# Kernel tuning notes

Hardware: AMD Instinct MI355X
Metric: run time of the kernel (lower is better)

Reference implementation:

```python
import jax, jax.numpy as jnp
import numpy as np

B, N, F_, H, K_IN, K = 2, 768, 128, 128, 2, 2
TAU = 0.66


def setup_inputs() -> dict:
    key = jax.random.key(0)
    ks = jax.random.split(key, 8)
    s = lambda fan: 1.0 / np.sqrt(fan)
    X = jax.random.normal(ks[0], (B, N, F_), jnp.float32)
    # edge_feat RezeroMLP: Linear(F,H) -> act -> Linear(H,H)
    ef_w1 = jax.random.normal(ks[1], (F_, H), jnp.float32) * s(F_)
    ef_b1 = jnp.zeros((H,), jnp.float32)
    ef_w2 = jax.random.normal(ks[2], (H, H), jnp.float32) * s(H)
    ef_b2 = jnp.zeros((H,), jnp.float32)
    # rezero gate (init 0 in module; use small nonzero so the branch is exercised)
    gate = jnp.asarray(0.1, jnp.float32)
    # score_mlp RezeroMLP: Linear(k_in,H) -> ReLU -> Linear(H,k)
    sm_w1 = jax.random.normal(ks[3], (K_IN, H), jnp.float32) * s(K_IN)
    sm_b1 = jnp.zeros((H,), jnp.float32)
    sm_w2 = jax.random.normal(ks[4], (H, K), jnp.float32) * s(H)
    sm_b2 = jnp.zeros((K,), jnp.float32)
    # pre-sampled standard Gumbel noise for gumbel_softmax
    u = jax.random.uniform(ks[5], (B, N, N, K), jnp.float32, minval=1e-6, maxval=1.0 - 1e-6)
    gumbel = -jnp.log(-jnp.log(u))
    return {"X": X, "ef_w1": ef_w1, "ef_b1": ef_b1, "ef_w2": ef_w2, "ef_b2": ef_b2,
            "gate": gate, "sm_w1": sm_w1, "sm_b1": sm_b1, "sm_w2": sm_w2, "sm_b2": sm_b2,
            "gumbel": gumbel}


def reference(X, ef_w1, ef_b1, ef_w2, ef_b2, gate, sm_w1, sm_b1, sm_w2, sm_b2, gumbel):
    # edge_feat MLP: [B,N,F] -> [B,N,H]
    feats = jax.nn.relu(X @ ef_w1 + ef_b1) @ ef_w2 + ef_b2
    D = H // K_IN
    Xact = feats.reshape(B, N, D, K_IN)
    Xskip = X.reshape(B, N, D, K_IN)  # feat_dim == hidden_dim, proj is None
    Xc = (Xskip + gate * Xact).transpose(0, 3, 1, 2)  # [B,k_in,N,D]
    # pairwise outer product ('prod' scoring): [B,N,N,k_in]
    prod = jnp.einsum('bkid,bkjd->bijk', Xc, Xc)
    # per-edge score MLP: k_in -> H -> k
    scores = jax.nn.relu(prod @ sm_w1 + sm_b1) @ sm_w2 + sm_b2  # [B,N,N,k]
    logits = scores - jnp.max(scores, axis=-1, keepdims=True)
    # gumbel-softmax, hard (straight-through)
    y_soft = jax.nn.softmax((logits + gumbel) / TAU, axis=-1)
    y_hard = jax.nn.one_hot(jnp.argmax(y_soft, axis=-1), K, dtype=y_soft.dtype)
    y = y_hard + y_soft - jax.lax.stop_gradient(y_soft)
    # A = y @ zo with zo = [0,1,...]: probability/one-hot mass of 'edge' states
    zo = jnp.ones((K,), y.dtype).at[0].set(0.0)
    A = y @ zo  # [B,N,N]
    # zero diagonal and symmetrize via upper triangle
    Au = jnp.triu(A, 1)
    return Au + jnp.swapaxes(Au, -1, -2)
```

## Files before the change

### kernel.cpp

```cpp
#include <hip/hip_runtime.h>

#define BB 2
#define NN 768
#define FF 128
#define HH 128
#define TS 32
#define LST 68
#define NT (NN / TS)
#define NPAIR (NT * (NT + 1) / 2)
#define EROWS 2
#define THR 4e-3f

__device__ __forceinline__
double edge_exact_f64(const double* __restrict__ Xc, const double* __restrict__ wpack,
                      int b, int i, int j, double init) {
    const double* xi0 = Xc + ((size_t)(b * 2 + 0) * NN + i) * 64;
    const double* xj0 = Xc + ((size_t)(b * 2 + 0) * NN + j) * 64;
    const double* xi1 = Xc + ((size_t)(b * 2 + 1) * NN + i) * 64;
    const double* xj1 = Xc + ((size_t)(b * 2 + 1) * NN + j) * 64;
    double p0 = 0.0, p1 = 0.0;
#pragma unroll 4
    for (int d2 = 0; d2 < 32; ++d2) {
        double2 a0 = *(const double2*)&xi0[2 * d2];
        double2 b0 = *(const double2*)&xj0[2 * d2];
        double2 a1 = *(const double2*)&xi1[2 * d2];
        double2 b1 = *(const double2*)&xj1[2 * d2];
        p0 = fma(a0.y, b0.y, fma(a0.x, b0.x, p0));
        p1 = fma(a1.y, b1.y, fma(a1.x, b1.x, p1));
    }
    double m = init;
#pragma unroll 8
    for (int c = 0; c < HH; ++c) {
        double2 wab = *(const double2*)&wpack[4 * c];
        double2 wbw = *(const double2*)&wpack[4 * c + 2];
        double tt = fma(p1, wab.y, fma(p0, wab.x, wbw.x));
        tt = fmax(tt, 0.0);
        m = fma(tt, wbw.y, m);
    }
    return m;
}

__global__ __launch_bounds__(128)
void edgefeat_kernel(const float* __restrict__ X,
                     const float* __restrict__ w1, const float* __restrict__ b1,
                     const float* __restrict__ w2, const float* __restrict__ b2,
                     const float* __restrict__ gatep,
                     const float* __restrict__ sm_w1, const float* __restrict__ sm_b1,
                     const float* __restrict__ sm_w2,
                     double* __restrict__ Xc, float* __restrict__ Xcf,
                     double* __restrict__ wpack, float4* __restrict__ wpackf) {
    __shared__ float  Xs[EROWS][FF];
    __shared__ double Hs[EROWS][HH];
    const int h = threadIdx.x;
    const int row0 = blockIdx.x * EROWS;
    for (int r = 0; r < EROWS; ++r) Xs[r][h] = X[(size_t)(row0 + r) * FF + h];
    if (blockIdx.x == 0) {
        double a  = (double)sm_w1[h];
        double bq = (double)sm_w1[HH + h];
        double be = (double)sm_b1[h];
        double wd = (double)sm_w2[2 * h + 1] - (double)sm_w2[2 * h + 0];
        wpack[4 * h + 0] = a;  wpack[4 * h + 1] = bq;
        wpack[4 * h + 2] = be; wpack[4 * h + 3] = wd;
        wpackf[h] = make_float4((float)a, (float)bq, (float)be, (float)wd);
    }
    __syncthreads();
    double acc[EROWS];
    double bb = (double)b1[h];
    for (int r = 0; r < EROWS; ++r) acc[r] = bb;
    for (int f = 0; f < FF; ++f) {
        double w = (double)w1[f * HH + h];
        for (int r = 0; r < EROWS; ++r) acc[r] = fma((double)Xs[r][f], w, acc[r]);
    }
    for (int r = 0; r < EROWS; ++r) Hs[r][h] = acc[r] > 0.0 ? acc[r] : 0.0;
    __syncthreads();
    bb = (double)b2[h];
    for (int r = 0; r < EROWS; ++r) acc[r] = bb;
    for (int c = 0; c < HH; ++c) {
        double w = (double)w2[c * HH + h];
        for (int r = 0; r < EROWS; ++r) acc[r] = fma(Hs[r][c], w, acc[r]);
    }
    const double gate = (double)gatep[0];
    const int k = h & 1, d = h >> 1;
    const int b = row0 / NN;
    const int i0 = row0 % NN;
    for (int r = 0; r < EROWS; ++r) {
        double v = (double)Xs[r][h] + gate * acc[r];
        size_t idx = (((size_t)(b * 2 + k)) * NN + (i0 + r)) * 64 + d;
        Xc[idx]  = v;
        Xcf[idx] = (float)v;
    }
}

__global__ __launch_bounds__(512, 6)
void edge_decide_kernel(const double* __restrict__ Xc,
                        const float* __restrict__ Xcf,
                        const double* __restrict__ wpack,
                        const float4* __restrict__ wpackf,
                        const float* __restrict__ sm_b2,
                        const float* __restrict__ gumbel,
                        float* __restrict__ out) {
    __shared__ float  Ai[2][TS][LST];
    __shared__ float  Aj[2][TS][LST];
    __shared__ float  As[TS][TS + 1];
    const int b = blockIdx.y;
    const int t = blockIdx.x;
    int ti = (int)((49.0 - sqrt(2401.0 - 8.0 * (double)t)) * 0.5);
    int base = ti * (49 - ti) / 2;
    if (t < base) { --ti; base = ti * (49 - ti) / 2; }
    else { int nb = (ti + 1) * (48 - ti) / 2; if (t >= nb) { ++ti; base = nb; } }
    const int tj = t - base + ti;
    const int tid = threadIdx.x;
    const int i0 = ti * TS, j0 = tj * TS;

    for (int q = 0; q < 4; ++q) {
        int flat = tid + 512 * q;
        int dp = flat & 31;
        int r  = (flat >> 5) & 31;
        int k  = flat >> 10;
        size_t rowbase = ((size_t)(b * 2 + k)) * NN;
        *(float2*)&Ai[k][r][2 * dp] = *(const float2*)&Xcf[(rowbase + i0 + r) * 64 + 2 * dp];
        *(float2*)&Aj[k][r][2 * dp] = *(const float2*)&Xcf[(rowbase + j0 + r) * 64 + 2 * dp];
    }

    const int s  = tid & 1;
    const int e  = tid >> 1;
    const int rh = e >> 4;
    const int ch = e & 15;
    const int r0 = rh, r1 = rh + 16;
    const int c0 = 2 * ch, c1 = c0 + 1;
    const int lr  = (s == 0) ? r0 : r1;
    const int gr  = i0 + lr;
    const int gj0 = j0 + c0, gj1 = j0 + c1;

    float4 gv = *(const float4*)&gumbel[(((size_t)b * NN + gr) * NN + gj0) * 2];
    __syncthreads();

    float p000 = 0.f, p001 = 0.f, p010 = 0.f, p011 = 0.f;
    float p100 = 0.f, p101 = 0.f, p110 = 0.f, p111 = 0.f;
#pragma unroll
    for (int it = 0; it < 8; ++it) {
        const int d4 = (s + 2 * it) * 4;
        float4 a00 = *(const float4*)&Ai[0][r0][d4];
        float4 a01 = *(const float4*)&Ai[0][r1][d4];
        float4 a10 = *(const float4*)&Ai[1][r0][d4];
        float4 a11 = *(const float4*)&Ai[1][r1][d4];
        float4 b00 = *(const float4*)&Aj[0][c0][d4];
        float4 b01 = *(const float4*)&Aj[0][c1][d4];
        float4 b10 = *(const float4*)&Aj[1][c0][d4];
        float4 b11 = *(const float4*)&Aj[1][c1][d4];
        p000 = fmaf(a00.w, b00.w, fmaf(a00.z, b00.z, fmaf(a00.y, b00.y, fmaf(a00.x, b00.x, p000))));
        p001 = fmaf(a00.w, b01.w, fmaf(a00.z, b01.z, fmaf(a00.y, b01.y, fmaf(a00.x, b01.x, p001))));
        p010 = fmaf(a01.w, b00.w, fmaf(a01.z, b00.z, fmaf(a01.y, b00.y, fmaf(a01.x, b00.x, p010))));
        p011 = fmaf(a01.w, b01.w, fmaf(a01.z, b01.z, fmaf(a01.y, b01.y, fmaf(a01.x, b01.x, p011))));
        p100 = fmaf(a10.w, b10.w, fmaf(a10.z, b10.z, fmaf(a10.y, b10.y, fmaf(a10.x, b10.x, p100))));
        p101 = fmaf(a10.w, b11.w, fmaf(a10.z, b11.z, fmaf(a10.y, b11.y, fmaf(a10.x, b11.x, p101))));
        p110 = fmaf(a11.w, b10.w, fmaf(a11.z, b10.z, fmaf(a11.y, b10.y, fmaf(a11.x, b10.x, p110))));
        p111 = fmaf(a11.w, b11.w, fmaf(a11.z, b11.z, fmaf(a11.y, b11.y, fmaf(a11.x, b11.x, p111))));
    }
    p000 += __shfl_xor(p000, 1); p001 += __shfl_xor(p001, 1);
    p010 += __shfl_xor(p010, 1); p011 += __shfl_xor(p011, 1);
    p100 += __shfl_xor(p100, 1); p101 += __shfl_xor(p101, 1);
    p110 += __shfl_xor(p110, 1); p111 += __shfl_xor(p111, 1);

    const float pa0 = (s == 0) ? p000 : p010;
    const float pa1 = (s == 0) ? p100 : p110;
    const float pb0 = (s == 0) ? p001 : p011;
    const float pb1 = (s == 0) ? p101 : p111;

    float ma = 0.f, mb = 0.f;
#pragma unroll 1
    for (int c = 0; c < HH; c += 8) {
        float4 w[8];
#pragma unroll
        for (int u = 0; u < 8; ++u) w[u] = wpackf[c + u];
#pragma unroll
        for (int u = 0; u < 8; ++u) {
            float tt;
            tt = fmaf(pa1, w[u].y, fmaf(pa0, w[u].x, w[u].z)); tt = fmaxf(tt, 0.f); ma = fmaf(tt, w[u].w, ma);
            tt = fmaf(pb1, w[u].y, fmaf(pb0, w[u].x, w[u].z)); tt = fmaxf(tt, 0.f); mb = fmaf(tt, w[u].w, mb);
        }
    }

    const double bd = (double)sm_b2[1] - (double)sm_b2[0];
    double ia = bd + ((double)gv.y - (double)gv.x);
    double ib = bd + ((double)gv.w - (double)gv.z);
    float fa = ma + (float)ia;
    float fb = mb + (float)ib;
    float Aa = fa > 0.f ? 1.f : 0.f;
    float Ab = fb > 0.f ? 1.f : 0.f;
    if (__builtin_expect(fminf(fabsf(fa), fabsf(fb)) < THR, 0)) {
        if (fabsf(fa) < THR) Aa = edge_exact_f64(Xc, wpack, b, gr, gj0, ia) > 0.0 ? 1.f : 0.f;
        if (fabsf(fb) < THR) Ab = edge_exact_f64(Xc, wpack, b, gr, gj1, ib) > 0.0 ? 1.f : 0.f;
    }
    As[lr][c0] = Aa; As[lr][c1] = Ab;
    __syncthreads();

    if (ti != tj) {
        *(float2*)&out[((size_t)b * NN + gr) * NN + gj0] = make_float2(Aa, Ab);
        float2 tv = make_float2(As[c0][lr], As[c1][lr]);
        *(float2*)&out[((size_t)b * NN + j0 + lr) * NN + i0 + c0] = tv;
    } else {
        float v0 = (lr < c0) ? Aa : ((lr > c0) ? As[c0][lr] : 0.0f);
        float v1 = (lr < c1) ? Ab : ((lr > c1) ? As[c1][lr] : 0.0f);
        *(float2*)&out[((size_t)b * NN + gr) * NN + gj0] = make_float2(v0, v1);
    }
}

extern "C" void kernel_launch(void* const* d_in, const int* in_sizes, int n_in,
                              void* d_out, int out_size, void* d_ws, size_t ws_size,
                              hipStream_t stream) {
    const float* X      = (const float*)d_in[0];
    const float* ef_w1  = (const float*)d_in[1];
    const float* ef_b1  = (const float*)d_in[2];
    const float* ef_w2  = (const float*)d_in[3];
    const float* ef_b2  = (const float*)d_in[4];
    const float* gate   = (const float*)d_in[5];
    const float* sm_w1  = (const float*)d_in[6];
    const float* sm_b1  = (const float*)d_in[7];
    const float* sm_w2  = (const float*)d_in[8];
    const float* sm_b2  = (const float*)d_in[9];
    const float* gumbel = (const float*)d_in[10];
    float* out = (float*)d_out;

    double* Xc     = (double*)d_ws;
    double* wpack  = Xc + (size_t)BB * 2 * NN * 64;
    float4* wpackf = (float4*)(wpack + 4 * HH);
    float*  Xcf    = (float*)(wpackf + HH);

    edgefeat_kernel<<<BB * NN / EROWS, 128, 0, stream>>>(
        X, ef_w1, ef_b1, ef_w2, ef_b2, gate, sm_w1, sm_b1, sm_w2, Xc, Xcf, wpack, wpackf);
    dim3 grid(NPAIR, BB);
    edge_decide_kernel<<<grid, 512, 0, stream>>>(Xc, Xcf, wpack, wpackf, sm_b2, gumbel, out);
}
```

Baseline: 118.7 us.

## Split edge-feature MLP reduction across two thread halves; widen loads; double-buffer weight reads

The edge-feature kernel now launches 256 threads per block. Each half accumulates half of the F (or H) reduction in double precision, and the partial sums are combined through shared memory. This shortens the serial FP64 dot-product chain per thread, at the cost of extra shared memory and synchronisation. In the decide kernel, tile loads become float4 instead of float2, and the score-MLP weight reads are software-pipelined with two register buffers so the next group's loads overlap the current group's FMAs.

```diff
diff --git a/kernel.cpp b/kernel.cpp
--- a/kernel.cpp
+++ b/kernel.cpp
@@ -40,7 +40,7 @@
     return m;
 }
 
-__global__ __launch_bounds__(128)
+__global__ __launch_bounds__(256)
 void edgefeat_kernel(const float* __restrict__ X,
                      const float* __restrict__ w1, const float* __restrict__ b1,
                      const float* __restrict__ w2, const float* __restrict__ b2,
@@ -50,11 +50,14 @@
                      double* __restrict__ Xc, float* __restrict__ Xcf,
                      double* __restrict__ wpack, float4* __restrict__ wpackf) {
     __shared__ float  Xs[EROWS][FF];
+    __shared__ double Hp[2][EROWS][HH];
     __shared__ double Hs[EROWS][HH];
-    const int h = threadIdx.x;
+    const int tid = threadIdx.x;
+    const int h  = tid & 127;
+    const int kh = tid >> 7;
     const int row0 = blockIdx.x * EROWS;
-    for (int r = 0; r < EROWS; ++r) Xs[r][h] = X[(size_t)(row0 + r) * FF + h];
-    if (blockIdx.x == 0) {
+    Xs[kh][h] = X[(size_t)(row0 + kh) * FF + h];
+    if (blockIdx.x == 0 && kh == 0) {
         double a  = (double)sm_w1[h];
         double bq = (double)sm_w1[HH + h];
         double be = (double)sm_b1[h];
@@ -64,30 +67,45 @@
         wpackf[h] = make_float4((float)a, (float)bq, (float)be, (float)wd);
     }
     __syncthreads();
-    double acc[EROWS];
-    double bb = (double)b1[h];
-    for (int r = 0; r < EROWS; ++r) acc[r] = bb;
-    for (int f = 0; f < FF; ++f) {
+    const int f0 = kh * 64;
+    double acc0 = (kh == 0) ? (double)b1[h] : 0.0;
+    double acc1 = acc0;
+    for (int f = f0; f < f0 + 64; ++f) {
         double w = (double)w1[f * HH + h];
-        for (int r = 0; r < EROWS; ++r) acc[r] = fma((double)Xs[r][f], w, acc[r]);
-    }
-    for (int r = 0; r < EROWS; ++r) Hs[r][h] = acc[r] > 0.0 ? acc[r] : 0.0;
-    __syncthreads();
-    bb = (double)b2[h];
-    for (int r = 0; r < EROWS; ++r) acc[r] = bb;
-    for (int c = 0; c < HH; ++c) {
+        acc0 = fma((double)Xs[0][f], w, acc0);
+        acc1 = fma((double)Xs[1][f], w, acc1);
+    }
+    Hp[kh][0][h] = acc0; Hp[kh][1][h] = acc1;
+    __syncthreads();
+    if (kh == 0) {
+        double v0 = Hp[0][0][h] + Hp[1][0][h];
+        double v1 = Hp[0][1][h] + Hp[1][1][h];
+        Hs[0][h] = v0 > 0.0 ? v0 : 0.0;
+        Hs[1][h] = v1 > 0.0 ? v1 : 0.0;
+    }
+    __syncthreads();
+    acc0 = (kh == 0) ? (double)b2[h] : 0.0;
+    acc1 = acc0;
+    for (int c = f0; c < f0 + 64; ++c) {
         double w = (double)w2[c * HH + h];
-        for (int r = 0; r < EROWS; ++r) acc[r] = fma(Hs[r][c], w, acc[r]);
-    }
-    const double gate = (double)gatep[0];
-    const int k = h & 1, d = h >> 1;
-    const int b = row0 / NN;
-    const int i0 = row0 % NN;
-    for (int r = 0; r < EROWS; ++r) {
-        double v = (double)Xs[r][h] + gate * acc[r];
-        size_t idx = (((size_t)(b * 2 + k)) * NN + (i0 + r)) * 64 + d;
-        Xc[idx]  = v;
-        Xcf[idx] = (float)v;
+        acc0 = fma(Hs[0][c], w, acc0);
+        acc1 = fma(Hs[1][c], w, acc1);
+    }
+    Hp[kh][0][h] = acc0; Hp[kh][1][h] = acc1;
+    __syncthreads();
+    if (kh == 0) {
+        const double gate = (double)gatep[0];
+        const int k = h & 1, d = h >> 1;
+        const int b = row0 / NN;
+        const int i0 = row0 % NN;
+#pragma unroll
+        for (int r = 0; r < EROWS; ++r) {
+            double a = Hp[0][r][h] + Hp[1][r][h];
+            double v = (double)Xs[r][h] + gate * a;
+            size_t idx = (((size_t)(b * 2 + k)) * NN + (i0 + r)) * 64 + d;
+            Xc[idx]  = v;
+            Xcf[idx] = (float)v;
+        }
     }
 }
 
@@ -112,14 +130,14 @@
     const int tid = threadIdx.x;
     const int i0 = ti * TS, j0 = tj * TS;
 
-    for (int q = 0; q < 4; ++q) {
+    for (int q = 0; q < 2; ++q) {
         int flat = tid + 512 * q;
-        int dp = flat & 31;
-        int r  = (flat >> 5) & 31;
-        int k  = flat >> 10;
+        int d4 = flat & 15;
+        int r  = (flat >> 4) & 31;
+        int k  = flat >> 9;
         size_t rowbase = ((size_t)(b * 2 + k)) * NN;
-        *(float2*)&Ai[k][r][2 * dp] = *(const float2*)&Xcf[(rowbase + i0 + r) * 64 + 2 * dp];
-        *(float2*)&Aj[k][r][2 * dp] = *(const float2*)&Xcf[(rowbase + j0 + r) * 64 + 2 * dp];
+        *(float4*)&Ai[k][r][4 * d4] = *(const float4*)&Xcf[(rowbase + i0 + r) * 64 + 4 * d4];
+        *(float4*)&Aj[k][r][4 * d4] = *(const float4*)&Xcf[(rowbase + j0 + r) * 64 + 4 * d4];
     }
 
     const int s  = tid & 1;
@@ -168,16 +186,28 @@
     const float pb1 = (s == 0) ? p101 : p111;
 
     float ma = 0.f, mb = 0.f;
+    float4 wA[8], wB[8];
+#pragma unroll
+    for (int u = 0; u < 8; ++u) wA[u] = wpackf[u];
 #pragma unroll 1
-    for (int c = 0; c < HH; c += 8) {
-        float4 w[8];
-#pragma unroll
-        for (int u = 0; u < 8; ++u) w[u] = wpackf[c + u];
+    for (int cg = 0; cg < 8; ++cg) {
+        const float4* nxt1 = wpackf + (16 * cg + 8);
+#pragma unroll
+        for (int u = 0; u < 8; ++u) wB[u] = nxt1[u];
 #pragma unroll
         for (int u = 0; u < 8; ++u) {
             float tt;
-            tt = fmaf(pa1, w[u].y, fmaf(pa0, w[u].x, w[u].z)); tt = fmaxf(tt, 0.f); ma = fmaf(tt, w[u].w, ma);
-            tt = fmaf(pb1, w[u].y, fmaf(pb0, w[u].x, w[u].z)); tt = fmaxf(tt, 0.f); mb = fmaf(tt, w[u].w, mb);
+            tt = fmaf(pa1, wA[u].y, fmaf(pa0, wA[u].x, wA[u].z)); tt = fmaxf(tt, 0.f); ma = fmaf(tt, wA[u].w, ma);
+            tt = fmaf(pb1, wA[u].y, fmaf(pb0, wA[u].x, wA[u].z)); tt = fmaxf(tt, 0.f); mb = fmaf(tt, wA[u].w, mb);
+        }
+        const float4* nxt2 = wpackf + ((cg < 7) ? (16 * cg + 16) : 0);
+#pragma unroll
+        for (int u = 0; u < 8; ++u) wA[u] = nxt2[u];
+#pragma unroll
+        for (int u = 0; u < 8; ++u) {
+            float tt;
+            tt = fmaf(pa1, wB[u].y, fmaf(pa0, wB[u].x, wB[u].z)); tt = fmaxf(tt, 0.f); ma = fmaf(tt, wB[u].w, ma);
+            tt = fmaf(pb1, wB[u].y, fmaf(pb0, wB[u].x, wB[u].z)); tt = fmaxf(tt, 0.f); mb = fmaf(tt, wB[u].w, mb);
         }
     }
 
@@ -227,7 +257,7 @@
     float4* wpackf = (float4*)(wpack + 4 * HH);
     float*  Xcf    = (float*)(wpackf + HH);
 
-    edgefeat_kernel<<<BB * NN / EROWS, 128, 0, stream>>>(
+    edgefeat_kernel<<<BB * NN / EROWS, 256, 0, stream>>>(
         X, ef_w1, ef_b1, ef_w2, ef_b2, gate, sm_w1, sm_b1, sm_w2, Xc, Xcf, wpack, wpackf);
     dim3 grid(NPAIR, BB);
     edge_decide_kernel<<<grid, 512, 0, stream>>>(Xc, Xcf, wpack, wpackf, sm_b2, gumbel, out);
```

After: 116.8 us. About the same (-1.6%).
